# Kernel optimization log

Measured on AMD Instinct MI355X. Metric: run time of the kernel, lower is better.

Reference implementation:

```python
import jax, jax.numpy as jnp
import numpy as np

B, T, C = 1, 2048, 2048
H = 16
DN, DR, DV = 128, 64, 128          # qk_nope_head_dim, qk_rope_head_dim, v_head_dim
QKD = DN + DR                      # 192
RQ, RKV = 1536, 512                # q_lora_rank, kv_lora_rank
EPS = 1e-6
SCALE = QKD ** -0.5


def rmsnorm(v, w):
    return v * jax.lax.rsqrt(jnp.mean(v * v, axis=-1, keepdims=True) + EPS) * w


def rope(x, freqs):
    # x: (B, T, H, d), freqs: (T, d//2) angles. Consecutive-pair complex rotation
    # matching torch view_as_complex(x.reshape(..., -1, 2)) * freqs.
    cos = jnp.cos(freqs)[None, :, None, :]
    sin = jnp.sin(freqs)[None, :, None, :]
    xp = x.reshape(*x.shape[:-1], -1, 2)
    xr, xi = xp[..., 0], xp[..., 1]
    outr = xr * cos - xi * sin
    outi = xr * sin + xi * cos
    return jnp.stack([outr, outi], axis=-1).reshape(x.shape)


def setup_inputs() -> dict:
    key = jax.random.key(0)
    ks = jax.random.split(key, 8)
    s = 0.02
    pos = jnp.arange(T, dtype=jnp.float32)
    inv = 1.0 / (10000.0 ** (jnp.arange(0, DR, 2, dtype=jnp.float32) / DR))  # (DR/2,)
    freqs = pos[:, None] * inv[None, :]  # (T, DR/2) rotation angles
    return {
        "x": jax.random.normal(ks[0], (B, T, C), jnp.float32),
        "freqs": freqs,
        "wq_a": jax.random.normal(ks[1], (RQ, C), jnp.float32) * s,
        "bq_a": jnp.zeros((RQ,), jnp.float32),
        "q_norm_w": jnp.ones((RQ,), jnp.float32),
        "wq_b": jax.random.normal(ks[2], (H * QKD, RQ), jnp.float32) * s,
        "bq_b": jnp.zeros((H * QKD,), jnp.float32),
        "wkv_a": jax.random.normal(ks[3], (RKV + DR, C), jnp.float32) * s,
        "bkv_a": jnp.zeros((RKV + DR,), jnp.float32),
        "kv_norm_w": jnp.ones((RKV,), jnp.float32),
        "wkv_b": jax.random.normal(ks[4], (H * (DN + DV), RKV), jnp.float32) * s,
        "bkv_b": jnp.zeros((H * (DN + DV),), jnp.float32),
        "wo": jax.random.normal(ks[5], (C, C), jnp.float32) * s,
        "bo": jnp.zeros((C,), jnp.float32),
        "prefill": 1,
        "cache_pos": 0,
    }


def reference(x, freqs, wq_a, bq_a, q_norm_w, wq_b, bq_b, wkv_a, bkv_a,
              kv_norm_w, wkv_b, bkv_b, wo, bo, prefill, cache_pos):
    # --- low-rank Q projection ---
    q_lat = rmsnorm(x @ wq_a.T + bq_a, q_norm_w)                 # (B,T,RQ)
    q = (q_lat @ wq_b.T + bq_b).reshape(B, T, H, QKD)
    q_nope, q_pe = q[..., :DN], q[..., DN:]
    q_pe = rope(q_pe, freqs)

    # --- low-rank KV projection ---
    kvpe = x @ wkv_a.T + bkv_a                                   # (B,T,RKV+DR)
    kv_lat, k_pe = kvpe[..., :RKV], kvpe[..., RKV:]
    k_pe = rope(k_pe[:, :, None, :], freqs)                      # (B,T,1,DR)
    kvb = (rmsnorm(kv_lat, kv_norm_w) @ wkv_b.T + bkv_b).reshape(B, T, H, DN + DV)
    k_nope, v = kvb[..., :DN], kvb[..., DN:]

    q = jnp.concatenate([q_nope, q_pe], axis=-1)                 # (B,T,H,QKD)
    k = jnp.concatenate([k_nope, jnp.broadcast_to(k_pe, (B, T, H, DR))], axis=-1)

    # --- causal SDPA (prefill: cache holds exactly the current T tokens) ---
    scores = jnp.einsum('bthd,bshd->bhts', q, k) * SCALE         # (B,H,T,T)
    mask = jnp.tril(jnp.ones((T, T), dtype=bool))
    scores = jnp.where(mask, scores, -jnp.inf)
    att = jax.nn.softmax(scores, axis=-1)
    y = jnp.einsum('bhts,bshd->bthd', att, v).reshape(B, T, C)
    return y @ wo.T + bo
```

## Files before the change

kernel.cpp:

```cpp
#include <hip/hip_runtime.h>
#include <hip/hip_bf16.h>


#define T_DIM 2048
#define H_DIM 16
#define SCALE_F 0.07216878364870322f
#define EPS_F 1e-6f
#define NEG_INF (-3.402823466e38f)

typedef __attribute__((ext_vector_type(8))) short short8;
typedef __attribute__((ext_vector_type(4))) float f32x4;
typedef __attribute__((address_space(3))) char lds_char;
typedef const __attribute__((address_space(1))) char glb_char;

__device__ inline void st_out(float* p, float v) { *p = v; }
__device__ inline void st_out(__hip_bfloat16* p, float v) { *p = __float2bfloat16(v); }

__global__ void cast_bf16_kernel(const float* __restrict__ src,
                                 __hip_bfloat16* __restrict__ dst,
                                 int n4_src, int n4_dst) {
    int i = blockIdx.x * 256 + threadIdx.x;
    if (i >= n4_dst) return;
    float4 v = make_float4(0.f, 0.f, 0.f, 0.f);
    if (i < n4_src) v = ((const float4*)src)[i];
    dst[4 * i + 0] = __float2bfloat16(v.x);
    dst[4 * i + 1] = __float2bfloat16(v.y);
    dst[4 * i + 2] = __float2bfloat16(v.z);
    dst[4 * i + 3] = __float2bfloat16(v.w);
}

__global__ void cast_wa_kernel(const float* __restrict__ wq_a,
                               const float* __restrict__ wkv_a,
                               __hip_bfloat16* __restrict__ WA) {
    int i = blockIdx.x * 256 + threadIdx.x;
    if (i >= 1114112) return;
    float4 v = make_float4(0.f, 0.f, 0.f, 0.f);
    if (i < 786432) v = ((const float4*)wq_a)[i];
    else if (i - 786432 < 294912) v = ((const float4*)wkv_a)[i - 786432];
    __hip_bfloat16* dst = WA + 4 * (size_t)i;
    dst[0] = __float2bfloat16(v.x);
    dst[1] = __float2bfloat16(v.y);
    dst[2] = __float2bfloat16(v.z);
    dst[3] = __float2bfloat16(v.w);
}

__global__ void bias_ab_kernel(const float* __restrict__ bq_a,
                               const float* __restrict__ bkv_a,
                               float* __restrict__ dst) {
    int i = blockIdx.x * 256 + threadIdx.x;
    if (i >= 2176) return;
    dst[i] = (i < 1536) ? bq_a[i] : ((i - 1536) < 576 ? bkv_a[i - 1536] : 0.f);
}

template <typename OT>
__global__ __launch_bounds__(512) void gemm_mfma_kernel(
    const __hip_bfloat16* __restrict__ A, int lda,
    const __hip_bfloat16* __restrict__ W, int ldw,
    const float* __restrict__ bias,
    OT* __restrict__ C, int ldc,
    float* __restrict__ C2, int ldc2, int splitN, int K) {
    __shared__ __hip_bfloat16 As[2][128 * 64];
    __shared__ __hip_bfloat16 Bs[2][128 * 64];
    const int tid = threadIdx.x;
    const int w = tid >> 6, lane = tid & 63, qd = lane >> 4, lx = lane & 15;

    const int nwg = gridDim.x * gridDim.y;
    const int o = blockIdx.y * gridDim.x + blockIdx.x;
    const int qx = nwg >> 3, rx = nwg & 7;
    const int xcd = o & 7, idx = o >> 3;
    const int neu = (xcd < rx ? xcd * (qx + 1) : rx * (qx + 1) + (xcd - rx) * qx) + idx;
    const int rowB = (neu / gridDim.x) * 128, colB = (neu % gridDim.x) * 128;

    const int wr = (w >> 1) * 32, wc = (w & 1) * 64;

    f32x4 acc[2][4];
#pragma unroll
    for (int i = 0; i < 2; ++i)
#pragma unroll
        for (int j = 0; j < 4; ++j) acc[i][j] = (f32x4)(0.f);

    auto stage = [&](int buf, int k0) {
#pragma unroll
        for (int it = 0; it < 2; ++it) {
            const int g = tid + it * 512;
            const int row = g >> 3, s = g & 7;
            const int sc = (s ^ (row & 7)) * 8;
            const __hip_bfloat16* ga = A + (size_t)(rowB + row) * lda + k0 + sc;
            __builtin_amdgcn_global_load_lds((glb_char*)ga,
                (lds_char*)((char*)&As[buf][0] + (size_t)g * 16), 16, 0, 0);
            const __hip_bfloat16* gb = W + (size_t)(colB + row) * ldw + k0 + sc;
            __builtin_amdgcn_global_load_lds((glb_char*)gb,
                (lds_char*)((char*)&Bs[buf][0] + (size_t)g * 16), 16, 0, 0);
        }
    };

    stage(0, 0);
    __syncthreads();
    int cur = 0;
    const int swz = (lx & 7) << 4;
    for (int k0 = 0; k0 < K; k0 += 64) {
        if (k0 + 64 < K) stage(cur ^ 1, k0 + 64);

#pragma unroll
        for (int kk = 0; kk < 2; ++kk) {
            short8 a[2], b[4];
#pragma unroll
            for (int rt = 0; rt < 2; ++rt)
                a[rt] = *(const short8*)((char*)&As[cur][0]
                    + (size_t)(wr + rt * 16 + lx) * 128 + ((kk * 64 + qd * 16) ^ swz));
#pragma unroll
            for (int ct = 0; ct < 4; ++ct)
                b[ct] = *(const short8*)((char*)&Bs[cur][0]
                    + (size_t)(wc + ct * 16 + lx) * 128 + ((kk * 64 + qd * 16) ^ swz));
#pragma unroll
            for (int rt = 0; rt < 2; ++rt)
#pragma unroll
                for (int ct = 0; ct < 4; ++ct)
                    acc[rt][ct] = __builtin_amdgcn_mfma_f32_16x16x32_bf16(a[rt], b[ct], acc[rt][ct], 0, 0, 0);
        }
        __syncthreads();
        cur ^= 1;
    }

    const bool second = (C2 != nullptr) && (colB >= splitN);
#pragma unroll
    for (int rt = 0; rt < 2; ++rt)
#pragma unroll
        for (int j = 0; j < 4; ++j) {
            const int row = rowB + wr + rt * 16 + 4 * qd + j;
#pragma unroll
            for (int ct = 0; ct < 4; ++ct) {
                const int col = colB + wc + ct * 16 + lx;
                const float v = acc[rt][ct][j] + bias[col];
                if (second) C2[(size_t)row * ldc2 + (col - splitN)] = v;
                else        st_out(&C[(size_t)row * ldc + col], v);
            }
        }
}

__global__ void rmsnorm_kernel(const float* __restrict__ in, __hip_bfloat16* __restrict__ outp,
                               const float* __restrict__ w,
                               int D, int in_stride, int out_stride) {
    const int row = blockIdx.x;
    const float* p = in + (size_t)row * in_stride;
    __hip_bfloat16* o = outp + (size_t)row * out_stride;
    const int tid = threadIdx.x;
    float ss = 0.f;
    for (int i = tid; i < D; i += 256) { float v = p[i]; ss += v * v; }
    __shared__ float red[256];
    red[tid] = ss;
    __syncthreads();
    for (int off = 128; off > 0; off >>= 1) {
        if (tid < off) red[tid] += red[tid + off];
        __syncthreads();
    }
    const float scale = rsqrtf(red[0] / (float)D + EPS_F);
    for (int i = tid; i < D; i += 256)
        o[i] = __float2bfloat16(p[i] * scale * w[i]);
}

__global__ void rmsnorm_rope_kv_kernel(const float* __restrict__ kvpe,
                                       __hip_bfloat16* __restrict__ kv_lat_bf,
                                       const float* __restrict__ w,
                                       const float* __restrict__ freqs,
                                       __hip_bfloat16* __restrict__ kpe) {
    const int row = blockIdx.x;
    const float* p = kvpe + (size_t)row * 640;
    const int tid = threadIdx.x;
    float v0 = p[tid], v1 = p[tid + 256];
    __shared__ float red[256];
    red[tid] = v0 * v0 + v1 * v1;
    __syncthreads();
    for (int off = 128; off > 0; off >>= 1) {
        if (tid < off) red[tid] += red[tid + off];
        __syncthreads();
    }
    const float scale = rsqrtf(red[0] / 512.f + EPS_F);
    __hip_bfloat16* o = kv_lat_bf + (size_t)row * 512;
    o[tid]       = __float2bfloat16(v0 * scale * w[tid]);
    o[tid + 256] = __float2bfloat16(v1 * scale * w[tid + 256]);
    if (tid < 32) {
        const float f = freqs[row * 32 + tid];
        const float c = cosf(f), s = sinf(f);
        const float xr = p[512 + 2 * tid], xi = p[512 + 2 * tid + 1];
        kpe[(size_t)row * 64 + 2 * tid]     = __float2bfloat16(xr * c - xi * s);
        kpe[(size_t)row * 64 + 2 * tid + 1] = __float2bfloat16(xr * s + xi * c);
    }
}

__global__ void rope_q_bf_kernel(__hip_bfloat16* __restrict__ qb,
                                 const float* __restrict__ freqs) {
    const int idx = blockIdx.x * 256 + threadIdx.x;
    const int t = idx >> 9;
    const int h = (idx >> 5) & 15;
    const int i = idx & 31;
    const float f = freqs[t * 32 + i];
    const float c = cosf(f), s = sinf(f);
    __hip_bfloat16* p = qb + (size_t)t * 3072 + h * 192 + 128 + 2 * i;
    const float xr = __bfloat162float(p[0]), xi = __bfloat162float(p[1]);
    p[0] = __float2bfloat16(xr * c - xi * s);
    p[1] = __float2bfloat16(xr * s + xi * c);
}

__global__ void pack_vT_kernel(const __hip_bfloat16* __restrict__ kvb,
                               __hip_bfloat16* __restrict__ vT) {
    const int t0 = blockIdx.x * 64;
    const int h = blockIdx.y;
    const int tid = threadIdx.x;
    __shared__ __hip_bfloat16 Ls[64][136];
#pragma unroll
    for (int it = 0; it < 4; ++it) {
        int c = tid + 256 * it;
        int i = c >> 4, part = c & 15;
        *(uint4*)&Ls[i][part * 8] =
            *(const uint4*)(kvb + (size_t)(t0 + i) * 4096 + h * 256 + 128 + part * 8);
    }
    __syncthreads();
#pragma unroll
    for (int it = 0; it < 32; ++it) {
        int c = tid + 256 * it;
        int d = c >> 6, i = c & 63;
        vT[((size_t)(h * 128 + d)) * 2048 + t0 + i] = Ls[i][d];
    }
}

__global__ __launch_bounds__(256) void attn_mfma_kernel(
    const __hip_bfloat16* __restrict__ q,
    const __hip_bfloat16* __restrict__ kv,
    const __hip_bfloat16* __restrict__ kpe,
    const __hip_bfloat16* __restrict__ vT,
    __hip_bfloat16* __restrict__ y) {
    const int o = blockIdx.x;
    const int xcd = o & 7, slot = o >> 3;
    const int h  = xcd * 2 + (slot & 1);
    const int qt = 31 - (slot >> 1);
    const int q0 = qt * 64;
    const int tid = threadIdx.x;
    const int w = tid >> 6, lane = tid & 63, qd = lane >> 4, lx = lane & 15;

    __shared__ __hip_bfloat16 KsB[64 * 192];
    __shared__ __hip_bfloat16 VsB[128 * 64];
    __shared__ __hip_bfloat16 Ps[4][16][72];

#define KS_ADDR(row, boff) ((char*)KsB + (size_t)(row) * 384 + ((boff) ^ (((row) & 7) << 4)))
#define VS_ADDR(row, boff) ((char*)VsB + (size_t)(row) * 128 + ((boff) ^ (((row) & 7) << 4)))

    short8 qf[6];
    {
        const __hip_bfloat16* qrow =
            q + (size_t)(q0 + 16 * w + lx) * 3072 + h * 192 + qd * 8;
#pragma unroll
        for (int kc = 0; kc < 6; ++kc)
            qf[kc] = *(const short8*)(qrow + kc * 32);
    }

    f32x4 O[8];
#pragma unroll
    for (int i = 0; i < 8; ++i) O[i] = (f32x4)(0.f);
    float mrow[4], lrow[4];
#pragma unroll
    for (int j = 0; j < 4; ++j) { mrow[j] = NEG_INF; lrow[j] = 0.f; }

    const short8 vone = (short8)(short)0x3F80;

    uint4 k0r, k1r, k2r, k3r, pe0r, pe1r, v0r, v1r, v2r, v3r;
    const __hip_bfloat16* kvh = kv + h * 256;
    const __hip_bfloat16* vTh = vT + (size_t)h * 128 * 2048;

#define PREFETCH(S0)                                                               \
    do {                                                                           \
        const size_t kk_ = (size_t)(S0) + (tid >> 4);                              \
        const int kp_ = (tid & 15) * 8;                                            \
        k0r = *(const uint4*)(kvh + (kk_ +  0) * 4096 + kp_);                      \
        k1r = *(const uint4*)(kvh + (kk_ + 16) * 4096 + kp_);                      \
        k2r = *(const uint4*)(kvh + (kk_ + 32) * 4096 + kp_);                      \
        k3r = *(const uint4*)(kvh + (kk_ + 48) * 4096 + kp_);                      \
        const size_t pk_ = (size_t)(S0) + (tid >> 3);                              \
        const int pp_ = (tid & 7) * 8;                                             \
        pe0r = *(const uint4*)(kpe + (pk_ +  0) * 64 + pp_);                       \
        pe1r = *(const uint4*)(kpe + (pk_ + 32) * 64 + pp_);                       \
        const __hip_bfloat16* vp_ = vTh + ((size_t)(tid >> 3)) * 2048 + (S0) + pp_;\
        v0r = *(const uint4*)(vp_ + 0 * 65536);                                    \
        v1r = *(const uint4*)(vp_ + 1 * 65536);                                    \
        v2r = *(const uint4*)(vp_ + 2 * 65536);                                    \
        v3r = *(const uint4*)(vp_ + 3 * 65536);                                    \
    } while (0)

    PREFETCH(0);

    for (int s0 = 0; s0 <= q0 + 63; s0 += 64) {
        __syncthreads();
        {
            const int kr_ = tid >> 4, kb_ = (tid & 15) * 16;
            *(uint4*)KS_ADDR(kr_ +  0, kb_) = k0r;
            *(uint4*)KS_ADDR(kr_ + 16, kb_) = k1r;
            *(uint4*)KS_ADDR(kr_ + 32, kb_) = k2r;
            *(uint4*)KS_ADDR(kr_ + 48, kb_) = k3r;
            const int pr_ = tid >> 3, pb_ = (tid & 7) * 16;
            *(uint4*)KS_ADDR(pr_ +  0, 256 + pb_) = pe0r;
            *(uint4*)KS_ADDR(pr_ + 32, 256 + pb_) = pe1r;
            *(uint4*)VS_ADDR(pr_ +  0, pb_) = v0r;
            *(uint4*)VS_ADDR(pr_ + 32, pb_) = v1r;
            *(uint4*)VS_ADDR(pr_ + 64, pb_) = v2r;
            *(uint4*)VS_ADDR(pr_ + 96, pb_) = v3r;
        }
        __syncthreads();

        if (s0 + 64 <= q0) PREFETCH(s0 + 64);

        f32x4 S[4];
#pragma unroll
        for (int nt = 0; nt < 4; ++nt) S[nt] = (f32x4)(0.f);
        __builtin_amdgcn_s_setprio(1);
#pragma unroll
        for (int kc = 0; kc < 6; ++kc) {
            short8 a = qf[kc];
#pragma unroll
            for (int nt = 0; nt < 4; ++nt) {
                short8 b = *(const short8*)KS_ADDR(nt * 16 + lx, kc * 64 + qd * 16);
                S[nt] = __builtin_amdgcn_mfma_f32_16x16x32_bf16(a, b, S[nt], 0, 0, 0);
            }
        }
        __builtin_amdgcn_s_setprio(0);

        float sv[4][4];
#pragma unroll
        for (int nt = 0; nt < 4; ++nt) {
            int col = s0 + nt * 16 + lx;
#pragma unroll
            for (int j = 0; j < 4; ++j) {
                int row = q0 + 16 * w + 4 * qd + j;
                float v = S[nt][j] * SCALE_F;
                sv[nt][j] = (col > row) ? NEG_INF : v;
            }
        }

        float pmax[4];
#pragma unroll
        for (int j = 0; j < 4; ++j)
            pmax[j] = fmaxf(fmaxf(sv[0][j], sv[1][j]), fmaxf(sv[2][j], sv[3][j]));
        const bool need = !__all((pmax[0] <= mrow[0] + 8.f) &&
                                 (pmax[1] <= mrow[1] + 8.f) &&
                                 (pmax[2] <= mrow[2] + 8.f) &&
                                 (pmax[3] <= mrow[3] + 8.f));
        if (need) {
            float al[4];
#pragma unroll
            for (int j = 0; j < 4; ++j) {
                float rm = pmax[j];
#pragma unroll
                for (int msk = 1; msk < 16; msk <<= 1)
                    rm = fmaxf(rm, __shfl_xor(rm, msk));
                const float mn = fmaxf(mrow[j], rm);
                al[j] = __expf(mrow[j] - mn);
                mrow[j] = mn;
                lrow[j] *= al[j];
            }
#pragma unroll
            for (int nt = 0; nt < 8; ++nt)
#pragma unroll
                for (int j = 0; j < 4; ++j) O[nt][j] *= al[j];
        }
#pragma unroll
        for (int nt = 0; nt < 4; ++nt)
#pragma unroll
            for (int j = 0; j < 4; ++j) {
                float p = __expf(sv[nt][j] - mrow[j]);
                Ps[w][4 * qd + j][nt * 16 + lx] = __float2bfloat16(p);
            }

        asm volatile("s_waitcnt lgkmcnt(0)" ::: "memory");

        f32x4 lacc = (f32x4)(0.f);
        __builtin_amdgcn_s_setprio(1);
#pragma unroll
        for (int kc2 = 0; kc2 < 2; ++kc2) {
            short8 pa = *(const short8*)&Ps[w][lx][kc2 * 32 + qd * 8];
#pragma unroll
            for (int nt = 0; nt < 8; ++nt) {
                short8 vb = *(const short8*)VS_ADDR(nt * 16 + lx, kc2 * 64 + qd * 16);
                O[nt] = __builtin_amdgcn_mfma_f32_16x16x32_bf16(pa, vb, O[nt], 0, 0, 0);
            }
            lacc = __builtin_amdgcn_mfma_f32_16x16x32_bf16(pa, vone, lacc, 0, 0, 0);
        }
        __builtin_amdgcn_s_setprio(0);

#pragma unroll
        for (int j = 0; j < 4; ++j) lrow[j] += lacc[j];
    }
#undef PREFETCH
#undef KS_ADDR
#undef VS_ADDR

#pragma unroll
    for (int j = 0; j < 4; ++j) {
        const float inv = 1.f / lrow[j];
        const int t = q0 + 16 * w + 4 * qd + j;
        __hip_bfloat16* yr = y + (size_t)t * 2048 + h * 128 + lx;
#pragma unroll
        for (int nt = 0; nt < 8; ++nt) yr[nt * 16] = __float2bfloat16(O[nt][j] * inv);
    }
}

extern "C" void kernel_launch(void* const* d_in, const int* in_sizes, int n_in,
                              void* d_out, int out_size, void* d_ws, size_t ws_size,
                              hipStream_t stream) {
    const float* x         = (const float*)d_in[0];
    const float* freqs     = (const float*)d_in[1];
    const float* wq_a      = (const float*)d_in[2];
    const float* bq_a      = (const float*)d_in[3];
    const float* q_norm_w  = (const float*)d_in[4];
    const float* wq_b      = (const float*)d_in[5];
    const float* bq_b      = (const float*)d_in[6];
    const float* wkv_a     = (const float*)d_in[7];
    const float* bkv_a     = (const float*)d_in[8];
    const float* kv_norm_w = (const float*)d_in[9];
    const float* wkv_b     = (const float*)d_in[10];
    const float* bkv_b     = (const float*)d_in[11];
    const float* wo        = (const float*)d_in[12];
    const float* bo        = (const float*)d_in[13];
    float* out = (float*)d_out;

    char* p = (char*)d_ws;
    float* q_lat = (float*)p;                        p += (size_t)2048 * 1536 * 4;
    float* kvpe  = (float*)p;                        p += (size_t)2048 * 640 * 4;
    __hip_bfloat16* x_bf      = (__hip_bfloat16*)p;  p += (size_t)2048 * 2048 * 2;
    __hip_bfloat16* q_lat_bf  = (__hip_bfloat16*)p;  p += (size_t)2048 * 1536 * 2;
    __hip_bfloat16* qb_bf     = (__hip_bfloat16*)p;  p += (size_t)2048 * 3072 * 2;
    __hip_bfloat16* kv_lat_bf = (__hip_bfloat16*)p;  p += (size_t)2048 * 512 * 2;
    __hip_bfloat16* kvb_bf    = (__hip_bfloat16*)p;  p += (size_t)2048 * 4096 * 2;
    __hip_bfloat16* kpe_bf    = (__hip_bfloat16*)p;  p += (size_t)2048 * 64 * 2;
    __hip_bfloat16* WA        = (__hip_bfloat16*)p;  p += (size_t)3072 * 1536 * 2;
    float* bias_ab = (float*)p;                      p += (size_t)2176 * 4;
    __hip_bfloat16* vT    = x_bf;
    __hip_bfloat16* yb_bf = (__hip_bfloat16*)q_lat;

    cast_bf16_kernel<<<4096, 256, 0, stream>>>(x, x_bf, 1048576, 1048576);
    cast_wa_kernel<<<4352, 256, 0, stream>>>(wq_a, wkv_a, WA);
    bias_ab_kernel<<<9, 256, 0, stream>>>(bq_a, bkv_a, bias_ab);
    gemm_mfma_kernel<float><<<dim3(17, 16), 512, 0, stream>>>(
        x_bf, 2048, WA, 2048, bias_ab, q_lat, 1536, kvpe, 640, 1536, 2048);
    rmsnorm_kernel<<<2048, 256, 0, stream>>>(q_lat, q_lat_bf, q_norm_w, 1536, 1536, 1536);
    cast_bf16_kernel<<<4608, 256, 0, stream>>>(wq_b, WA, 1179648, 1179648);
    gemm_mfma_kernel<__hip_bfloat16><<<dim3(24, 16), 512, 0, stream>>>(
        q_lat_bf, 1536, WA, 1536, bq_b, qb_bf, 3072, nullptr, 0, 1 << 30, 1536);
    rope_q_bf_kernel<<<4096, 256, 0, stream>>>(qb_bf, freqs);
    rmsnorm_rope_kv_kernel<<<2048, 256, 0, stream>>>(kvpe, kv_lat_bf, kv_norm_w, freqs, kpe_bf);
    cast_bf16_kernel<<<2048, 256, 0, stream>>>(wkv_b, WA, 524288, 524288);
    gemm_mfma_kernel<__hip_bfloat16><<<dim3(32, 16), 512, 0, stream>>>(
        kv_lat_bf, 512, WA, 512, bkv_b, kvb_bf, 4096, nullptr, 0, 1 << 30, 512);
    pack_vT_kernel<<<dim3(32, 16), 256, 0, stream>>>(kvb_bf, vT);
    attn_mfma_kernel<<<512, 256, 0, stream>>>(qb_bf, kvb_bf, kpe_bf, vT, yb_bf);
    cast_bf16_kernel<<<4096, 256, 0, stream>>>(wo, WA, 1048576, 1048576);
    gemm_mfma_kernel<float><<<dim3(16, 16), 512, 0, stream>>>(
        yb_bf, 2048, WA, 2048, bo, out, 2048, nullptr, 0, 1 << 30, 2048);
}
```

Baseline: 346.1 us.

## Merge cast kernels, fuse Q rope into GEMM epilogue, widen attention KV tiles

Merges the x, wq_a, wkv_a and wq_b casts plus the bias packing into one launch, and reorders the remaining weight casts. Q rope now runs in the GEMM epilogue using a lane shuffle, which removes the separate rope kernel's read-modify-write pass. The attention kernel stages 128 keys per sync and processes them as two 64-key halves, halving barrier and prefetch rounds. In exchange it uses more LDS and registers, which may lower occupancy, and the epilogue adds sin/cos work.

```diff
diff --git a/kernel.cpp b/kernel.cpp
--- a/kernel.cpp
+++ b/kernel.cpp
@@ -29,36 +29,53 @@
     dst[4 * i + 3] = __float2bfloat16(v.w);
 }
 
-__global__ void cast_wa_kernel(const float* __restrict__ wq_a,
-                               const float* __restrict__ wkv_a,
-                               __hip_bfloat16* __restrict__ WA) {
-    int i = blockIdx.x * 256 + threadIdx.x;
-    if (i >= 1114112) return;
+__global__ void megacast_kernel(const float* __restrict__ x,
+                                const float* __restrict__ wq_a,
+                                const float* __restrict__ wkv_a,
+                                const float* __restrict__ wq_b,
+                                const float* __restrict__ bq_a,
+                                const float* __restrict__ bkv_a,
+                                __hip_bfloat16* __restrict__ x_bf,
+                                __hip_bfloat16* __restrict__ A1,
+                                __hip_bfloat16* __restrict__ A2,
+                                float* __restrict__ bias_ab) {
+    const int i = blockIdx.x * 256 + threadIdx.x;
     float4 v = make_float4(0.f, 0.f, 0.f, 0.f);
-    if (i < 786432) v = ((const float4*)wq_a)[i];
-    else if (i - 786432 < 294912) v = ((const float4*)wkv_a)[i - 786432];
-    __hip_bfloat16* dst = WA + 4 * (size_t)i;
+    __hip_bfloat16* dst;
+    if (i < 1048576) {
+        v = ((const float4*)x)[i];            dst = x_bf + 4 * (size_t)i;
+    } else if (i < 1835008) {
+        int k = i - 1048576;
+        v = ((const float4*)wq_a)[k];         dst = A1 + 4 * (size_t)k;
+    } else if (i < 2162688) {
+        int k = i - 1835008;
+        if (k < 294912) v = ((const float4*)wkv_a)[k];
+        dst = A1 + (size_t)(786432 + k) * 4;
+    } else if (i < 3342336) {
+        int k = i - 2162688;
+        v = ((const float4*)wq_b)[k];         dst = A2 + 4 * (size_t)k;
+    } else if (i < 3342880) {
+        int k = i - 3342336;
+        float4 b = make_float4(0.f, 0.f, 0.f, 0.f);
+        if (k < 384) b = ((const float4*)bq_a)[k];
+        else if (k < 528) b = ((const float4*)bkv_a)[k - 384];
+        ((float4*)bias_ab)[k] = b;
+        return;
+    } else return;
     dst[0] = __float2bfloat16(v.x);
     dst[1] = __float2bfloat16(v.y);
     dst[2] = __float2bfloat16(v.z);
     dst[3] = __float2bfloat16(v.w);
 }
 
-__global__ void bias_ab_kernel(const float* __restrict__ bq_a,
-                               const float* __restrict__ bkv_a,
-                               float* __restrict__ dst) {
-    int i = blockIdx.x * 256 + threadIdx.x;
-    if (i >= 2176) return;
-    dst[i] = (i < 1536) ? bq_a[i] : ((i - 1536) < 576 ? bkv_a[i - 1536] : 0.f);
-}
-
-template <typename OT>
+template <typename OT, bool ROPE>
 __global__ __launch_bounds__(512) void gemm_mfma_kernel(
     const __hip_bfloat16* __restrict__ A, int lda,
     const __hip_bfloat16* __restrict__ W, int ldw,
     const float* __restrict__ bias,
     OT* __restrict__ C, int ldc,
-    float* __restrict__ C2, int ldc2, int splitN, int K) {
+    float* __restrict__ C2, int ldc2, int splitN, int K,
+    const float* __restrict__ freqs) {
     __shared__ __hip_bfloat16 As[2][128 * 64];
     __shared__ __hip_bfloat16 Bs[2][128 * 64];
     const int tid = threadIdx.x;
@@ -131,7 +148,18 @@
 #pragma unroll
             for (int ct = 0; ct < 4; ++ct) {
                 const int col = colB + wc + ct * 16 + lx;
-                const float v = acc[rt][ct][j] + bias[col];
+                float v = acc[rt][ct][j] + bias[col];
+                if constexpr (ROPE) {
+                    const float pv = __shfl_xor(v, 1);
+                    const int dm = col % 192;
+                    if (dm >= 128) {
+                        const int ii = (dm - 128) >> 1;
+                        const float f = freqs[row * 32 + ii];
+                        const float cc = cosf(f), ss = sinf(f);
+                        v = (lane & 1) ? (pv * ss + v * cc)
+                                       : (v * cc - pv * ss);
+                    }
+                }
                 if (second) C2[(size_t)row * ldc2 + (col - splitN)] = v;
                 else        st_out(&C[(size_t)row * ldc + col], v);
             }
@@ -188,20 +216,6 @@
     }
 }
 
-__global__ void rope_q_bf_kernel(__hip_bfloat16* __restrict__ qb,
-                                 const float* __restrict__ freqs) {
-    const int idx = blockIdx.x * 256 + threadIdx.x;
-    const int t = idx >> 9;
-    const int h = (idx >> 5) & 15;
-    const int i = idx & 31;
-    const float f = freqs[t * 32 + i];
-    const float c = cosf(f), s = sinf(f);
-    __hip_bfloat16* p = qb + (size_t)t * 3072 + h * 192 + 128 + 2 * i;
-    const float xr = __bfloat162float(p[0]), xi = __bfloat162float(p[1]);
-    p[0] = __float2bfloat16(xr * c - xi * s);
-    p[1] = __float2bfloat16(xr * s + xi * c);
-}
-
 __global__ void pack_vT_kernel(const __hip_bfloat16* __restrict__ kvb,
                                __hip_bfloat16* __restrict__ vT) {
     const int t0 = blockIdx.x * 64;
@@ -235,15 +249,16 @@
     const int h  = xcd * 2 + (slot & 1);
     const int qt = 31 - (slot >> 1);
     const int q0 = qt * 64;
+    const int NST = (qt >> 1) + 1;
     const int tid = threadIdx.x;
     const int w = tid >> 6, lane = tid & 63, qd = lane >> 4, lx = lane & 15;
 
-    __shared__ __hip_bfloat16 KsB[64 * 192];
-    __shared__ __hip_bfloat16 VsB[128 * 64];
+    __shared__ __hip_bfloat16 KsB[128 * 192];
+    __shared__ __hip_bfloat16 VsB[128 * 128];
     __shared__ __hip_bfloat16 Ps[4][16][72];
 
 #define KS_ADDR(row, boff) ((char*)KsB + (size_t)(row) * 384 + ((boff) ^ (((row) & 7) << 4)))
-#define VS_ADDR(row, boff) ((char*)VsB + (size_t)(row) * 128 + ((boff) ^ (((row) & 7) << 4)))
+#define VS_ADDR(row, boff) ((char*)VsB + (size_t)(row) * 256 + ((boff) ^ (((row) & 7) << 4)))
 
     short8 qf[6];
     {
@@ -263,7 +278,9 @@
 
     const short8 vone = (short8)(short)0x3F80;
 
-    uint4 k0r, k1r, k2r, k3r, pe0r, pe1r, v0r, v1r, v2r, v3r;
+    uint4 k0r, k1r, k2r, k3r, k4r, k5r, k6r, k7r;
+    uint4 pe0r, pe1r, pe2r, pe3r;
+    uint4 v0r, v1r, v2r, v3r, v4r, v5r, v6r, v7r;
     const __hip_bfloat16* kvh = kv + h * 256;
     const __hip_bfloat16* vTh = vT + (size_t)h * 128 * 2048;
 
@@ -271,124 +288,150 @@
     do {                                                                           \
         const size_t kk_ = (size_t)(S0) + (tid >> 4);                              \
         const int kp_ = (tid & 15) * 8;                                            \
-        k0r = *(const uint4*)(kvh + (kk_ +  0) * 4096 + kp_);                      \
-        k1r = *(const uint4*)(kvh + (kk_ + 16) * 4096 + kp_);                      \
-        k2r = *(const uint4*)(kvh + (kk_ + 32) * 4096 + kp_);                      \
-        k3r = *(const uint4*)(kvh + (kk_ + 48) * 4096 + kp_);                      \
+        k0r = *(const uint4*)(kvh + (kk_ +   0) * 4096 + kp_);                     \
+        k1r = *(const uint4*)(kvh + (kk_ +  16) * 4096 + kp_);                     \
+        k2r = *(const uint4*)(kvh + (kk_ +  32) * 4096 + kp_);                     \
+        k3r = *(const uint4*)(kvh + (kk_ +  48) * 4096 + kp_);                     \
+        k4r = *(const uint4*)(kvh + (kk_ +  64) * 4096 + kp_);                     \
+        k5r = *(const uint4*)(kvh + (kk_ +  80) * 4096 + kp_);                     \
+        k6r = *(const uint4*)(kvh + (kk_ +  96) * 4096 + kp_);                     \
+        k7r = *(const uint4*)(kvh + (kk_ + 112) * 4096 + kp_);                     \
         const size_t pk_ = (size_t)(S0) + (tid >> 3);                              \
         const int pp_ = (tid & 7) * 8;                                             \
         pe0r = *(const uint4*)(kpe + (pk_ +  0) * 64 + pp_);                       \
         pe1r = *(const uint4*)(kpe + (pk_ + 32) * 64 + pp_);                       \
-        const __hip_bfloat16* vp_ = vTh + ((size_t)(tid >> 3)) * 2048 + (S0) + pp_;\
-        v0r = *(const uint4*)(vp_ + 0 * 65536);                                    \
-        v1r = *(const uint4*)(vp_ + 1 * 65536);                                    \
-        v2r = *(const uint4*)(vp_ + 2 * 65536);                                    \
-        v3r = *(const uint4*)(vp_ + 3 * 65536);                                    \
+        pe2r = *(const uint4*)(kpe + (pk_ + 64) * 64 + pp_);                       \
+        pe3r = *(const uint4*)(kpe + (pk_ + 96) * 64 + pp_);                       \
+        const __hip_bfloat16* vp_ = vTh + (size_t)(tid >> 4) * 2048 + (S0) + kp_;  \
+        v0r = *(const uint4*)(vp_ + 0 * 32768);                                    \
+        v1r = *(const uint4*)(vp_ + 1 * 32768);                                    \
+        v2r = *(const uint4*)(vp_ + 2 * 32768);                                    \
+        v3r = *(const uint4*)(vp_ + 3 * 32768);                                    \
+        v4r = *(const uint4*)(vp_ + 4 * 32768);                                    \
+        v5r = *(const uint4*)(vp_ + 5 * 32768);                                    \
+        v6r = *(const uint4*)(vp_ + 6 * 32768);                                    \
+        v7r = *(const uint4*)(vp_ + 7 * 32768);                                    \
     } while (0)
 
+#define COMPUTE64(S0P, KOFF)                                                       \
+    do {                                                                           \
+        f32x4 S[4];                                                                \
+        _Pragma("unroll")                                                          \
+        for (int nt = 0; nt < 4; ++nt) S[nt] = (f32x4)(0.f);                       \
+        __builtin_amdgcn_s_setprio(1);                                             \
+        _Pragma("unroll")                                                          \
+        for (int kc = 0; kc < 6; ++kc) {                                           \
+            short8 a = qf[kc];                                                     \
+            _Pragma("unroll")                                                      \
+            for (int nt = 0; nt < 4; ++nt) {                                       \
+                short8 b = *(const short8*)KS_ADDR((KOFF) + nt * 16 + lx,          \
+                                                   kc * 64 + qd * 16);             \
+                S[nt] = __builtin_amdgcn_mfma_f32_16x16x32_bf16(a, b, S[nt], 0, 0, 0); \
+            }                                                                      \
+        }                                                                          \
+        __builtin_amdgcn_s_setprio(0);                                             \
+        float sv[4][4];                                                            \
+        _Pragma("unroll")                                                          \
+        for (int nt = 0; nt < 4; ++nt) {                                           \
+            int col = (S0P) + nt * 16 + lx;                                        \
+            _Pragma("unroll")                                                      \
+            for (int j = 0; j < 4; ++j) {                                          \
+                int row = q0 + 16 * w + 4 * qd + j;                                \
+                float v = S[nt][j] * SCALE_F;                                      \
+                sv[nt][j] = (col > row) ? NEG_INF : v;                             \
+            }                                                                      \
+        }                                                                          \
+        float pmax[4];                                                             \
+        _Pragma("unroll")                                                          \
+        for (int j = 0; j < 4; ++j)                                                \
+            pmax[j] = fmaxf(fmaxf(sv[0][j], sv[1][j]), fmaxf(sv[2][j], sv[3][j])); \
+        const bool need = !__all((pmax[0] <= mrow[0] + 8.f) &&                     \
+                                 (pmax[1] <= mrow[1] + 8.f) &&                     \
+                                 (pmax[2] <= mrow[2] + 8.f) &&                     \
+                                 (pmax[3] <= mrow[3] + 8.f));                      \
+        if (need) {                                                                \
+            float al[4];                                                           \
+            _Pragma("unroll")                                                      \
+            for (int j = 0; j < 4; ++j) {                                          \
+                float rm = pmax[j];                                                \
+                _Pragma("unroll")                                                  \
+                for (int msk = 1; msk < 16; msk <<= 1)                             \
+                    rm = fmaxf(rm, __shfl_xor(rm, msk));                           \
+                const float mn = fmaxf(mrow[j], rm);                               \
+                al[j] = __expf(mrow[j] - mn);                                      \
+                mrow[j] = mn;                                                      \
+                lrow[j] *= al[j];                                                  \
+            }                                                                      \
+            _Pragma("unroll")                                                      \
+            for (int nt = 0; nt < 8; ++nt)                                         \
+                _Pragma("unroll")                                                  \
+                for (int j = 0; j < 4; ++j) O[nt][j] *= al[j];                     \
+        }                                                                          \
+        _Pragma("unroll")                                                          \
+        for (int nt = 0; nt < 4; ++nt)                                             \
+            _Pragma("unroll")                                                      \
+            for (int j = 0; j < 4; ++j) {                                          \
+                float pp = __expf(sv[nt][j] - mrow[j]);                            \
+                Ps[w][4 * qd + j][nt * 16 + lx] = __float2bfloat16(pp);            \
+            }                                                                      \
+        asm volatile("s_waitcnt lgkmcnt(0)" ::: "memory");                         \
+        f32x4 lacc = (f32x4)(0.f);                                                 \
+        __builtin_amdgcn_s_setprio(1);                                             \
+        _Pragma("unroll")                                                          \
+        for (int kc2 = 0; kc2 < 2; ++kc2) {                                        \
+            short8 pa = *(const short8*)&Ps[w][lx][kc2 * 32 + qd * 8];             \
+            _Pragma("unroll")                                                      \
+            for (int nt = 0; nt < 8; ++nt) {                                       \
+                short8 vb = *(const short8*)VS_ADDR(nt * 16 + lx,                  \
+                                (KOFF) * 2 + kc2 * 64 + qd * 16);                  \
+                O[nt] = __builtin_amdgcn_mfma_f32_16x16x32_bf16(pa, vb, O[nt], 0, 0, 0); \
+            }                                                                      \
+            lacc = __builtin_amdgcn_mfma_f32_16x16x32_bf16(pa, vone, lacc, 0, 0, 0); \
+        }                                                                          \
+        __builtin_amdgcn_s_setprio(0);                                             \
+        _Pragma("unroll")                                                          \
+        for (int j = 0; j < 4; ++j) lrow[j] += lacc[j];                            \
+    } while (0)
+
     PREFETCH(0);
 
-    for (int s0 = 0; s0 <= q0 + 63; s0 += 64) {
+    for (int st = 0; st < NST; ++st) {
+        const int s0 = st * 128;
         __syncthreads();
         {
             const int kr_ = tid >> 4, kb_ = (tid & 15) * 16;
-            *(uint4*)KS_ADDR(kr_ +  0, kb_) = k0r;
-            *(uint4*)KS_ADDR(kr_ + 16, kb_) = k1r;
-            *(uint4*)KS_ADDR(kr_ + 32, kb_) = k2r;
-            *(uint4*)KS_ADDR(kr_ + 48, kb_) = k3r;
+            *(uint4*)KS_ADDR(kr_ +   0, kb_) = k0r;
+            *(uint4*)KS_ADDR(kr_ +  16, kb_) = k1r;
+            *(uint4*)KS_ADDR(kr_ +  32, kb_) = k2r;
+            *(uint4*)KS_ADDR(kr_ +  48, kb_) = k3r;
+            *(uint4*)KS_ADDR(kr_ +  64, kb_) = k4r;
+            *(uint4*)KS_ADDR(kr_ +  80, kb_) = k5r;
+            *(uint4*)KS_ADDR(kr_ +  96, kb_) = k6r;
+            *(uint4*)KS_ADDR(kr_ + 112, kb_) = k7r;
             const int pr_ = tid >> 3, pb_ = (tid & 7) * 16;
             *(uint4*)KS_ADDR(pr_ +  0, 256 + pb_) = pe0r;
             *(uint4*)KS_ADDR(pr_ + 32, 256 + pb_) = pe1r;
-            *(uint4*)VS_ADDR(pr_ +  0, pb_) = v0r;
-            *(uint4*)VS_ADDR(pr_ + 32, pb_) = v1r;
-            *(uint4*)VS_ADDR(pr_ + 64, pb_) = v2r;
-            *(uint4*)VS_ADDR(pr_ + 96, pb_) = v3r;
+            *(uint4*)KS_ADDR(pr_ + 64, 256 + pb_) = pe2r;
+            *(uint4*)KS_ADDR(pr_ + 96, 256 + pb_) = pe3r;
+            *(uint4*)VS_ADDR(kr_ +   0, kb_) = v0r;
+            *(uint4*)VS_ADDR(kr_ +  16, kb_) = v1r;
+            *(uint4*)VS_ADDR(kr_ +  32, kb_) = v2r;
+            *(uint4*)VS_ADDR(kr_ +  48, kb_) = v3r;
+            *(uint4*)VS_ADDR(kr_ +  64, kb_) = v4r;
+            *(uint4*)VS_ADDR(kr_ +  80, kb_) = v5r;
+            *(uint4*)VS_ADDR(kr_ +  96, kb_) = v6r;
+            *(uint4*)VS_ADDR(kr_ + 112, kb_) = v7r;
         }
         __syncthreads();
 
-        if (s0 + 64 <= q0) PREFETCH(s0 + 64);
-
-        f32x4 S[4];
-#pragma unroll
-        for (int nt = 0; nt < 4; ++nt) S[nt] = (f32x4)(0.f);
-        __builtin_amdgcn_s_setprio(1);
-#pragma unroll
-        for (int kc = 0; kc < 6; ++kc) {
-            short8 a = qf[kc];
-#pragma unroll
-            for (int nt = 0; nt < 4; ++nt) {
-                short8 b = *(const short8*)KS_ADDR(nt * 16 + lx, kc * 64 + qd * 16);
-                S[nt] = __builtin_amdgcn_mfma_f32_16x16x32_bf16(a, b, S[nt], 0, 0, 0);
-            }
-        }
-        __builtin_amdgcn_s_setprio(0);
-
-        float sv[4][4];
-#pragma unroll
-        for (int nt = 0; nt < 4; ++nt) {
-            int col = s0 + nt * 16 + lx;
-#pragma unroll
-            for (int j = 0; j < 4; ++j) {
-                int row = q0 + 16 * w + 4 * qd + j;
-                float v = S[nt][j] * SCALE_F;
-                sv[nt][j] = (col > row) ? NEG_INF : v;
-            }
-        }
-
-        float pmax[4];
-#pragma unroll
-        for (int j = 0; j < 4; ++j)
-            pmax[j] = fmaxf(fmaxf(sv[0][j], sv[1][j]), fmaxf(sv[2][j], sv[3][j]));
-        const bool need = !__all((pmax[0] <= mrow[0] + 8.f) &&
-                                 (pmax[1] <= mrow[1] + 8.f) &&
-                                 (pmax[2] <= mrow[2] + 8.f) &&
-                                 (pmax[3] <= mrow[3] + 8.f));
-        if (need) {
-            float al[4];
-#pragma unroll
-            for (int j = 0; j < 4; ++j) {
-                float rm = pmax[j];
-#pragma unroll
-                for (int msk = 1; msk < 16; msk <<= 1)
-                    rm = fmaxf(rm, __shfl_xor(rm, msk));
-                const float mn = fmaxf(mrow[j], rm);
-                al[j] = __expf(mrow[j] - mn);
-                mrow[j] = mn;
-                lrow[j] *= al[j];
-            }
-#pragma unroll
-            for (int nt = 0; nt < 8; ++nt)
-#pragma unroll
-                for (int j = 0; j < 4; ++j) O[nt][j] *= al[j];
-        }
-#pragma unroll
-        for (int nt = 0; nt < 4; ++nt)
-#pragma unroll
-            for (int j = 0; j < 4; ++j) {
-                float p = __expf(sv[nt][j] - mrow[j]);
-                Ps[w][4 * qd + j][nt * 16 + lx] = __float2bfloat16(p);
-            }
-
-        asm volatile("s_waitcnt lgkmcnt(0)" ::: "memory");
-
-        f32x4 lacc = (f32x4)(0.f);
-        __builtin_amdgcn_s_setprio(1);
-#pragma unroll
-        for (int kc2 = 0; kc2 < 2; ++kc2) {
-            short8 pa = *(const short8*)&Ps[w][lx][kc2 * 32 + qd * 8];
-#pragma unroll
-            for (int nt = 0; nt < 8; ++nt) {
-                short8 vb = *(const short8*)VS_ADDR(nt * 16 + lx, kc2 * 64 + qd * 16);
-                O[nt] = __builtin_amdgcn_mfma_f32_16x16x32_bf16(pa, vb, O[nt], 0, 0, 0);
-            }
-            lacc = __builtin_amdgcn_mfma_f32_16x16x32_bf16(pa, vone, lacc, 0, 0, 0);
-        }
-        __builtin_amdgcn_s_setprio(0);
-
-#pragma unroll
-        for (int j = 0; j < 4; ++j) lrow[j] += lacc[j];
+        if (st + 1 < NST) PREFETCH((st + 1) * 128);
+
+        COMPUTE64(s0, 0);
+        if (s0 < q0)
+            COMPUTE64(s0 + 64, 64);
     }
 #undef PREFETCH
+#undef COMPUTE64
 #undef KS_ADDR
 #undef VS_ADDR
 
@@ -430,28 +473,26 @@
     __hip_bfloat16* kv_lat_bf = (__hip_bfloat16*)p;  p += (size_t)2048 * 512 * 2;
     __hip_bfloat16* kvb_bf    = (__hip_bfloat16*)p;  p += (size_t)2048 * 4096 * 2;
     __hip_bfloat16* kpe_bf    = (__hip_bfloat16*)p;  p += (size_t)2048 * 64 * 2;
-    __hip_bfloat16* WA        = (__hip_bfloat16*)p;  p += (size_t)3072 * 1536 * 2;
+    __hip_bfloat16* A1        = (__hip_bfloat16*)p;  p += (size_t)3072 * 1536 * 2;
     float* bias_ab = (float*)p;                      p += (size_t)2176 * 4;
     __hip_bfloat16* vT    = x_bf;
     __hip_bfloat16* yb_bf = (__hip_bfloat16*)q_lat;
-
-    cast_bf16_kernel<<<4096, 256, 0, stream>>>(x, x_bf, 1048576, 1048576);
-    cast_wa_kernel<<<4352, 256, 0, stream>>>(wq_a, wkv_a, WA);
-    bias_ab_kernel<<<9, 256, 0, stream>>>(bq_a, bkv_a, bias_ab);
-    gemm_mfma_kernel<float><<<dim3(17, 16), 512, 0, stream>>>(
-        x_bf, 2048, WA, 2048, bias_ab, q_lat, 1536, kvpe, 640, 1536, 2048);
+    __hip_bfloat16* A2    = kvb_bf;
+
+    megacast_kernel<<<13059, 256, 0, stream>>>(x, wq_a, wkv_a, wq_b, bq_a, bkv_a,
+                                               x_bf, A1, A2, bias_ab);
+    gemm_mfma_kernel<float, false><<<dim3(17, 16), 512, 0, stream>>>(
+        x_bf, 2048, A1, 2048, bias_ab, q_lat, 1536, kvpe, 640, 1536, 2048, nullptr);
+    cast_bf16_kernel<<<2048, 256, 0, stream>>>(wkv_b, A1, 524288, 524288);
     rmsnorm_kernel<<<2048, 256, 0, stream>>>(q_lat, q_lat_bf, q_norm_w, 1536, 1536, 1536);
-    cast_bf16_kernel<<<4608, 256, 0, stream>>>(wq_b, WA, 1179648, 1179648);
-    gemm_mfma_kernel<__hip_bfloat16><<<dim3(24, 16), 512, 0, stream>>>(
-        q_lat_bf, 1536, WA, 1536, bq_b, qb_bf, 3072, nullptr, 0, 1 << 30, 1536);
-    rope_q_bf_kernel<<<4096, 256, 0, stream>>>(qb_bf, freqs);
+    gemm_mfma_kernel<__hip_bfloat16, true><<<dim3(24, 16), 512, 0, stream>>>(
+        q_lat_bf, 1536, A2, 1536, bq_b, qb_bf, 3072, nullptr, 0, 1 << 30, 1536, freqs);
     rmsnorm_rope_kv_kernel<<<2048, 256, 0, stream>>>(kvpe, kv_lat_bf, kv_norm_w, freqs, kpe_bf);
-    cast_bf16_kernel<<<2048, 256, 0, stream>>>(wkv_b, WA, 524288, 524288);
-    gemm_mfma_kernel<__hip_bfloat16><<<dim3(32, 16), 512, 0, stream>>>(
-        kv_lat_bf, 512, WA, 512, bkv_b, kvb_bf, 4096, nullptr, 0, 1 << 30, 512);
+    gemm_mfma_kernel<__hip_bfloat16, false><<<dim3(32, 16), 512, 0, stream>>>(
+        kv_lat_bf, 512, A1, 512, bkv_b, kvb_bf, 4096, nullptr, 0, 1 << 30, 512, nullptr);
+    cast_bf16_kernel<<<4096, 256, 0, stream>>>(wo, A1, 1048576, 1048576);
     pack_vT_kernel<<<dim3(32, 16), 256, 0, stream>>>(kvb_bf, vT);
     attn_mfma_kernel<<<512, 256, 0, stream>>>(qb_bf, kvb_bf, kpe_bf, vT, yb_bf);
-    cast_bf16_kernel<<<4096, 256, 0, stream>>>(wo, WA, 1048576, 1048576);
-    gemm_mfma_kernel<float><<<dim3(16, 16), 512, 0, stream>>>(
-        yb_bf, 2048, WA, 2048, bo, out, 2048, nullptr, 0, 1 << 30, 2048);
-}
+    gemm_mfma_kernel<float, false><<<dim3(16, 16), 512, 0, stream>>>(
+        yb_bf, 2048, A1, 2048, bo, out, 2048, nullptr, 0, 1 << 30, 2048, nullptr);
+}
```

New measurement: 355.1 us. 1.03x slower.
